# Performance work log

Measured on AMD Instinct MI355X. Metric: run time of the kernel, lower is better.

## Reference

```python
import jax, jax.numpy as jnp
import numpy as np

TOKEN_NUM = 8
GCN = 16          # group_channel_num = d_model
D_INNER = 32      # expand * d_model
D_STATE = 16
D_CONV = 4
DT_RANK = 1       # ceil(d_model / 16)
GROUPS = 4        # GroupNorm groups
EPS = 1e-5


def setup_inputs() -> dict:
    key = jax.random.key(0)
    ks = jax.random.split(key, 8)
    g = lambda k, shape, scale: jax.random.normal(k, shape, jnp.float32) * scale
    d = {}
    d["x"] = jax.random.normal(ks[0], (2, 128, 128, 128), jnp.float32)
    d["conv_w"] = g(ks[1], (128, 128, 3, 3), 0.03)
    d["conv_b"] = jnp.zeros((128,), jnp.float32)
    d["gn_w"] = jnp.ones((128,), jnp.float32)
    d["gn_b"] = jnp.zeros((128,), jnp.float32)
    d["in_proj_w"] = g(ks[2], (2 * D_INNER, GCN), 0.25)
    d["conv1d_w"] = g(ks[3], (D_INNER, 1, D_CONV), 0.3)
    d["conv1d_b"] = jnp.zeros((D_INNER,), jnp.float32)
    d["x_proj_w"] = g(ks[4], (DT_RANK + 2 * D_STATE, D_INNER), 0.18)
    d["dt_proj_w"] = g(ks[5], (D_INNER, DT_RANK), 1.0)
    d["dt_proj_b"] = jnp.full((D_INNER,), -2.0, jnp.float32)  # softplus -> small positive dt
    d["A_log"] = jnp.tile(jnp.log(jnp.arange(1, D_STATE + 1, dtype=jnp.float32)), (D_INNER, 1))
    d["D"] = jnp.ones((D_INNER,), jnp.float32)
    d["out_proj_w"] = g(ks[6], (GCN, D_INNER), 0.18)
    return d


def _mamba(seq, in_proj_w, conv1d_w, conv1d_b, x_proj_w, dt_proj_w, dt_proj_b, A_log, D, out_proj_w):
    # seq: (N, L, d_model)
    xz = jnp.einsum('nld,ed->nle', seq, in_proj_w)          # (N, L, 2*d_inner)
    xi, z = jnp.split(xz, 2, axis=-1)
    # causal depthwise conv1d over L, kernel D_CONV, then SiLU
    xc = jax.lax.conv_general_dilated(
        xi.transpose(0, 2, 1), conv1d_w, (1,), ((D_CONV - 1, 0),),
        dimension_numbers=('NCH', 'OIH', 'NCH'), feature_group_count=D_INNER)
    xc = jax.nn.silu((xc + conv1d_b[None, :, None]).transpose(0, 2, 1))  # (N, L, d_inner)
    xdbl = jnp.einsum('nld,ed->nle', xc, x_proj_w)          # (N, L, dt_rank+2*d_state)
    dt, Bm, Cm = jnp.split(xdbl, [DT_RANK, DT_RANK + D_STATE], axis=-1)
    dt = jax.nn.softplus(jnp.einsum('nlr,dr->nld', dt, dt_proj_w) + dt_proj_b)  # (N, L, d_inner)
    A = -jnp.exp(A_log)                                     # (d_inner, d_state)
    dA = jnp.exp(dt[..., None] * A)                         # (N, L, d_inner, d_state)
    dBx = dt[..., None] * Bm[:, :, None, :] * xc[..., None] # (N, L, d_inner, d_state)

    def step(h, inp):
        a, b, c = inp                                       # (N,d,s),(N,d,s),(N,s)
        h = a * h + b
        return h, jnp.sum(h * c[:, None, :], axis=-1)       # y_t: (N, d_inner)

    h0 = jnp.zeros((seq.shape[0], D_INNER, D_STATE), dA.dtype)
    _, ys = jax.lax.scan(step, h0, (dA.transpose(1, 0, 2, 3),
                                    dBx.transpose(1, 0, 2, 3),
                                    Cm.transpose(1, 0, 2)))
    ym = ys.transpose(1, 0, 2) + D * xc                     # skip connection D*x
    ym = ym * jax.nn.silu(z)                                # gate
    return jnp.einsum('nld,ed->nle', ym, out_proj_w)        # (N, L, d_model)


def reference(x, conv_w, conv_b, gn_w, gn_b, in_proj_w, conv1d_w, conv1d_b,
              x_proj_w, dt_proj_w, dt_proj_b, A_log, D, out_proj_w):
    B, C, H, W = x.shape
    # channels == channel_num so padding_feature is identity; 3x3 conv, pad 1
    y = jax.lax.conv_general_dilated(x, conv_w, (1, 1), ((1, 1), (1, 1)),
                                     dimension_numbers=('NCHW', 'OIHW', 'NCHW'))
    y = y + conv_b[None, :, None, None]
    seq = y.reshape(B * H * W, TOKEN_NUM, GCN)              # row-major view, matches torch .view
    out = _mamba(seq, in_proj_w, conv1d_w, conv1d_b, x_proj_w,
                 dt_proj_w, dt_proj_b, A_log, D, out_proj_w)
    xr = out.reshape(B, C, H, W)
    # GroupNorm(GROUPS, C) + SiLU
    g = xr.reshape(B, GROUPS, C // GROUPS, H, W)
    mu = g.mean((2, 3, 4), keepdims=True)
    var = g.var((2, 3, 4), keepdims=True)
    g = (g - mu) / jnp.sqrt(var + EPS)
    xp = g.reshape(B, C, H, W) * gn_w[None, :, None, None] + gn_b[None, :, None, None]
    xp = jax.nn.silu(xp)
    return x + xp
```

## Files before the change

kernel.cpp:

```cpp
#include <hip/hip_runtime.h>

typedef unsigned short USHORT;
typedef short short8 __attribute__((ext_vector_type(8)));
typedef float f32x4 __attribute__((ext_vector_type(4)));

__device__ __forceinline__ float fast_sig(float x) {
  return __builtin_amdgcn_rcpf(1.f + __builtin_amdgcn_exp2f(x * -1.442695041f));
}
__device__ __forceinline__ USHORT f2b(float f) {
  unsigned int u = __float_as_uint(f);
  unsigned int r = (u + 0x7fffu + ((u >> 16) & 1u)) >> 16;
  return (USHORT)r;
}
__device__ __forceinline__ void wave_lds_fence() {
  asm volatile("s_waitcnt lgkmcnt(0)" ::: "memory");
  __builtin_amdgcn_sched_barrier(0);
}

__global__ __launch_bounds__(256) void prep_k(
    const float* __restrict__ x, const float* __restrict__ cw,
    const float* __restrict__ w_in, const float* __restrict__ xpw,
    const float* __restrict__ wout,
    USHORT* __restrict__ xt_g, USHORT* __restrict__ wrep,
    USHORT* __restrict__ wbf) {
  const int tid = threadIdx.x;
  const int bid = blockIdx.x;
  if (bid < 2048) {
    __shared__ USHORT lt[128 * 18];
    const int cqi = bid & 7;
    const int h   = (bid >> 3) & 127;
    const int b   = bid >> 10;
    const int ci0 = cqi * 16;
#pragma unroll
    for (int it = 0; it < 2; ++it) {
      int task = it * 256 + tid;
      int ci = task >> 5;
      int wq = task & 31;
      float4 v = ((const float4*)(x + ((size_t)((b * 128 + ci0 + ci) * 128 + h)) * 128))[wq];
      lt[(wq * 4 + 0) * 18 + ci] = f2b(v.x);
      lt[(wq * 4 + 1) * 18 + ci] = f2b(v.y);
      lt[(wq * 4 + 2) * 18 + ci] = f2b(v.z);
      lt[(wq * 4 + 3) * 18 + ci] = f2b(v.w);
    }
    __syncthreads();
    unsigned int* dst = (unsigned int*)xt_g + ((size_t)((b * 128 + h) * 128)) * 64 + cqi * 8;
#pragma unroll
    for (int it = 0; it < 4; ++it) {
      int task = it * 256 + tid;
      int w = task >> 3;
      int p = task & 7;
      dst[(size_t)w * 64 + p] = *(const unsigned int*)&lt[w * 18 + 2 * p];
    }
  } else if (bid < 2624) {
    const int idx = (bid - 2048) * 256 + tid;
    const int t9 = idx % 9;
    const int r  = idx / 9;
    const int ci = r & 127;
    const int co = r >> 7;
    const int c  = ci >> 5;
    const int kg = (ci >> 3) & 3;
    const int j  = ci & 7;
    const int st = co >> 4;
    const int mm = co & 15;
    wrep[((c * 9 + t9) * 8 + st) * 512 + (kg * 16 + mm) * 8 + j] = f2b(cw[idx]);
  } else {
#pragma unroll
    for (int it = 0; it < 11; ++it) {
      int idx = it * 256 + tid;
      if (idx < 1024)      wbf[idx] = f2b(w_in[idx]);
      else if (idx < 2080) wbf[idx] = f2b(xpw[idx - 1024]);
      else if (idx < 2592) wbf[idx] = f2b(wout[idx - 2080]);
    }
  }
}

__global__ __launch_bounds__(512) void conv_mfma_k(
    const USHORT* __restrict__ xt_g, const USHORT* __restrict__ wrep,
    const float* __restrict__ cb, float* __restrict__ y) {
  __shared__ USHORT xt[3 * 136 * 136];

  const int tid = threadIdx.x;
  const int bid = blockIdx.x;
  const int h   = bid & 127;
  const int b   = bid >> 7;

  const int wv   = tid >> 6;
  const int lane = tid & 63;
  const int m    = lane & 15;
  const int kg   = lane >> 4;
  const int ch2  = wv & 1;
  const int co0w = ch2 * 64;
  const int ws0  = (wv >> 1) * 32;

  for (int it = 0; it < 13; ++it) {
    int task = it * 512 + tid;
    if (task < 6528) {
      int dh  = task / 2176;
      int rem = task - dh * 2176;
      int wl  = rem >> 4;
      int cq  = task & 15;
      int wg  = wl - 4;
      int hh  = h + dh - 1;
      uint4 v = make_uint4(0u, 0u, 0u, 0u);
      if (((unsigned)wg < 128u) && ((unsigned)hh < 128u))
        v = *(const uint4*)(xt_g + ((size_t)((b * 128 + hh) * 128 + wg)) * 128 + cq * 8);
      *(uint4*)&xt[(dh * 136 + wl) * 136 + cq * 8] = v;
    }
  }
  __syncthreads();

  f32x4 acc[4][2];
#pragma unroll
  for (int s = 0; s < 4; ++s)
#pragma unroll
    for (int ws = 0; ws < 2; ++ws) acc[s][ws] = (f32x4){0.f, 0.f, 0.f, 0.f};

  for (int c = 0; c < 4; ++c) {
#pragma unroll
    for (int t9 = 0; t9 < 9; ++t9) {
      const int kh = t9 / 3, kw = t9 - kh * 3;
      const USHORT* wbase = wrep + (size_t)(((c * 9 + t9) * 8 + ch2 * 4) * 512) + lane * 8;
      short8 a[4];
#pragma unroll
      for (int s = 0; s < 4; ++s)
        a[s] = *(const short8*)(wbase + s * 512);
#pragma unroll
      for (int ws = 0; ws < 2; ++ws) {
        short8 bf = *(const short8*)&xt[(kh * 136 + ws0 + ws * 16 + m + kw + 3) * 136 + c * 32 + kg * 8];
#pragma unroll
        for (int s = 0; s < 4; ++s)
          acc[s][ws] = __builtin_amdgcn_mfma_f32_16x16x32_bf16(a[s], bf, acc[s][ws], 0, 0, 0);
      }
    }
  }

#pragma unroll
  for (int s = 0; s < 4; ++s) {
#pragma unroll
    for (int ws = 0; ws < 2; ++ws) {
      const int w = ws0 + ws * 16 + m;
#pragma unroll
      for (int r = 0; r < 4; ++r) {
        const int co = co0w + s * 16 + kg * 4 + r;
        y[((size_t)((b * 128 + co) * 128 + h)) * 128 + w] = acc[s][ws][r] + cb[co];
      }
    }
  }
}

__global__ __launch_bounds__(256) void mamba_k(
    const float* __restrict__ y,
    const float* __restrict__ c1w, const float* __restrict__ c1b,
    const float* __restrict__ dtw, const float* __restrict__ dtb,
    const float* __restrict__ alog, const float* __restrict__ dvec,
    const USHORT* __restrict__ wbf,
    float* __restrict__ m, float* __restrict__ stats_part) {
  __shared__ float axs[64 * 36];
  __shared__ float azs[64 * 36];
  __shared__ USHORT ab[64 * 40];
  __shared__ float dt0s[64];
  __shared__ float Bs[64 * 16];
  __shared__ float Cs[64 * 16];
  __shared__ float reds[8];

  const int tid  = threadIdx.x;
  const int s    = tid >> 5;
  const int ch   = tid & 31;
  const int lane = tid & 63;
  const int wv   = tid >> 6;
  const int m15  = lane & 15;
  const int kg   = lane >> 4;

  const USHORT* w_inb = wbf;
  const USHORT* xpwb  = wbf + 1024;
  const USHORT* woutb = wbf + 2080;

  {
    short8 zero8 = (short8){0, 0, 0, 0, 0, 0, 0, 0};
    short8 a = zero8, b0 = zero8, b1 = zero8, b2 = zero8, b3 = zero8;
    if (kg < 2) {
      const int tok = wv * 16 + m15;
      const float* ya = y + (size_t)blockIdx.x * 1024 + (tok >> 3) * 128 + (tok & 7) * 16 + kg * 8;
      float4 f0 = *(const float4*)(ya);
      float4 f1 = *(const float4*)(ya + 4);
      a[0] = (short)f2b(f0.x); a[1] = (short)f2b(f0.y); a[2] = (short)f2b(f0.z); a[3] = (short)f2b(f0.w);
      a[4] = (short)f2b(f1.x); a[5] = (short)f2b(f1.y); a[6] = (short)f2b(f1.z); a[7] = (short)f2b(f1.w);
      b0 = *(const short8*)&w_inb[(0 * 16 + m15) * 16 + kg * 8];
      b1 = *(const short8*)&w_inb[(1 * 16 + m15) * 16 + kg * 8];
      b2 = *(const short8*)&w_inb[(2 * 16 + m15) * 16 + kg * 8];
      b3 = *(const short8*)&w_inb[(3 * 16 + m15) * 16 + kg * 8];
    }
    f32x4 zero = (f32x4){0.f, 0.f, 0.f, 0.f};
    f32x4 d0 = __builtin_amdgcn_mfma_f32_16x16x32_bf16(a, b0, zero, 0, 0, 0);
    f32x4 d1 = __builtin_amdgcn_mfma_f32_16x16x32_bf16(a, b1, zero, 0, 0, 0);
    f32x4 d2 = __builtin_amdgcn_mfma_f32_16x16x32_bf16(a, b2, zero, 0, 0, 0);
    f32x4 d3 = __builtin_amdgcn_mfma_f32_16x16x32_bf16(a, b3, zero, 0, 0, 0);
#pragma unroll
    for (int r = 0; r < 4; ++r) {
      const int tok = wv * 16 + kg * 4 + r;
      axs[tok * 36 + m15]      = d0[r];
      axs[tok * 36 + 16 + m15] = d1[r];
      azs[tok * 36 + m15]      = d2[r];
      azs[tok * 36 + 16 + m15] = d3[r];
    }
  }
  wave_lds_fence();

  const float4 cwv = *(const float4*)(c1w + ch * 4);
  const float cbr = c1b[ch];
  const float dwv = dtw[ch], dbv = dtb[ch], Dv = dvec[ch];
  float xc[8], zs[8];
  {
    float ax[8];
#pragma unroll
    for (int l = 0; l < 8; ++l) ax[l] = axs[(s * 8 + l) * 36 + ch];
#pragma unroll
    for (int l = 0; l < 8; ++l) {
      float a = fmaf(cwv.w, ax[l], cbr);
      if (l >= 1) a = fmaf(cwv.z, ax[l - 1], a);
      if (l >= 2) a = fmaf(cwv.y, ax[l - 2], a);
      if (l >= 3) a = fmaf(cwv.x, ax[l - 3], a);
      float sc = a * fast_sig(a);
      xc[l] = sc;
      ab[(s * 8 + l) * 40 + ch] = f2b(sc);
      float az = azs[(s * 8 + l) * 36 + ch];
      zs[l] = az * fast_sig(az);
    }
  }
  wave_lds_fence();

  {
    short8 a = *(const short8*)&ab[(wv * 16 + m15) * 40 + kg * 8];
    short8 b0 = *(const short8*)&xpwb[(0 * 16 + m15) * 32 + kg * 8];
    short8 b1 = *(const short8*)&xpwb[(1 * 16 + m15) * 32 + kg * 8];
    short8 b2;
    if (m15 == 0) b2 = *(const short8*)&xpwb[32 * 32 + kg * 8];
    else          b2 = (short8){0, 0, 0, 0, 0, 0, 0, 0};
    f32x4 zero = (f32x4){0.f, 0.f, 0.f, 0.f};
    f32x4 c0 = __builtin_amdgcn_mfma_f32_16x16x32_bf16(a, b0, zero, 0, 0, 0);
    f32x4 c1 = __builtin_amdgcn_mfma_f32_16x16x32_bf16(a, b1, zero, 0, 0, 0);
    f32x4 c2 = __builtin_amdgcn_mfma_f32_16x16x32_bf16(a, b2, zero, 0, 0, 0);
#pragma unroll
    for (int r = 0; r < 4; ++r) {
      const int tok = wv * 16 + kg * 4 + r;
      if (m15 == 0) {
        dt0s[tok] = c0[r];
        Bs[tok * 16 + 15] = c1[r];
        Cs[tok * 16 + 15] = c2[r];
      } else {
        Bs[tok * 16 + (m15 - 1)] = c0[r];
        Cs[tok * 16 + (m15 - 1)] = c1[r];
      }
    }
  }
  wave_lds_fence();

  float A2r[16];
#pragma unroll
  for (int q = 0; q < 4; ++q) {
    float4 av = ((const float4*)(alog + ch * 16))[q];
    A2r[q * 4 + 0] = -__builtin_amdgcn_exp2f(av.x * 1.442695041f) * 1.442695041f;
    A2r[q * 4 + 1] = -__builtin_amdgcn_exp2f(av.y * 1.442695041f) * 1.442695041f;
    A2r[q * 4 + 2] = -__builtin_amdgcn_exp2f(av.z * 1.442695041f) * 1.442695041f;
    A2r[q * 4 + 3] = -__builtin_amdgcn_exp2f(av.w * 1.442695041f) * 1.442695041f;
  }
  float hreg[16];
#pragma unroll
  for (int st = 0; st < 16; ++st) hreg[st] = 0.f;
#pragma unroll
  for (int l = 0; l < 8; ++l) {
    const int tok = s * 8 + l;
    float pre = fmaf(dt0s[tok], dwv, dbv);
    float t = __builtin_amdgcn_exp2f(pre * 1.442695041f);
    float dtl = 0.6931471806f * __builtin_amdgcn_logf(1.f + t);
    dtl = (pre > 20.f) ? pre : dtl;
    float dtxc = dtl * xc[l];
    float yl = 0.f;
#pragma unroll
    for (int q = 0; q < 4; ++q) {
      float4 bv = *(const float4*)&Bs[tok * 16 + q * 4];
      float4 cv = *(const float4*)&Cs[tok * 16 + q * 4];
      float aa;
      aa = __builtin_amdgcn_exp2f(dtl * A2r[q * 4 + 0]);
      hreg[q * 4 + 0] = fmaf(aa, hreg[q * 4 + 0], dtxc * bv.x);
      yl = fmaf(hreg[q * 4 + 0], cv.x, yl);
      aa = __builtin_amdgcn_exp2f(dtl * A2r[q * 4 + 1]);
      hreg[q * 4 + 1] = fmaf(aa, hreg[q * 4 + 1], dtxc * bv.y);
      yl = fmaf(hreg[q * 4 + 1], cv.y, yl);
      aa = __builtin_amdgcn_exp2f(dtl * A2r[q * 4 + 2]);
      hreg[q * 4 + 2] = fmaf(aa, hreg[q * 4 + 2], dtxc * bv.z);
      yl = fmaf(hreg[q * 4 + 2], cv.z, yl);
      aa = __builtin_amdgcn_exp2f(dtl * A2r[q * 4 + 3]);
      hreg[q * 4 + 3] = fmaf(aa, hreg[q * 4 + 3], dtxc * bv.w);
      yl = fmaf(hreg[q * 4 + 3], cv.w, yl);
    }
    ab[tok * 40 + ch] = f2b(fmaf(Dv, xc[l], yl) * zs[l]);
  }
  wave_lds_fence();

  float ls = 0.f, lq = 0.f;
  {
    short8 a2 = *(const short8*)&ab[(wv * 16 + m15) * 40 + kg * 8];
    short8 bo = *(const short8*)&woutb[m15 * 32 + kg * 8];
    f32x4 zero = (f32x4){0.f, 0.f, 0.f, 0.f};
    f32x4 o = __builtin_amdgcn_mfma_f32_16x16x32_bf16(a2, bo, zero, 0, 0, 0);
#pragma unroll
    for (int r = 0; r < 4; ++r) {
      const int tok = wv * 16 + kg * 4 + r;
      const int n   = blockIdx.x * 8 + (tok >> 3);
      const int l   = tok & 7;
      float v = o[r];
      m[(size_t)n * 128 + l * 16 + m15] = v;
      ls += v;
      lq = fmaf(v, v, lq);
    }
  }
#pragma unroll
  for (int off = 32; off > 0; off >>= 1) {
    ls += __shfl_down(ls, off);
    lq += __shfl_down(lq, off);
  }
  if (lane == 0) { reds[wv * 2] = ls; reds[wv * 2 + 1] = lq; }
  __syncthreads();
  if (tid == 0) {
    float S = reds[0] + reds[2] + reds[4] + reds[6];
    float Q = reds[1] + reds[3] + reds[5] + reds[7];
    int n0 = blockIdx.x * 8;
    int bb = n0 >> 14;
    int cc = (n0 >> 7) & 127;
    int gg = cc >> 5;
    float* line = stats_part + (blockIdx.x & 63) * 16;
    atomicAdd(&line[(bb * 4 + gg) * 2 + 0], S);
    atomicAdd(&line[(bb * 4 + gg) * 2 + 1], Q);
  }
}

__global__ __launch_bounds__(256) void gn_silu_k(
    const float* __restrict__ x,
    const float* __restrict__ gnw, const float* __restrict__ gnb,
    const float* __restrict__ stats_part, float* __restrict__ out) {
  __shared__ float sSQ[2];
  const int tid  = threadIdx.x;
  const int idx0 = (blockIdx.x * 256 + tid) * 4;
  const int bb = idx0 >> 21;
  const int cc = (idx0 >> 14) & 127;
  const int gg = cc >> 5;
  const int j2 = (bb * 4 + gg) * 2;

  if (tid < 64) {
    float s = stats_part[tid * 16 + j2];
    float q = stats_part[tid * 16 + j2 + 1];
#pragma unroll
    for (int off = 32; off > 0; off >>= 1) {
      s += __shfl_down(s, off);
      q += __shfl_down(q, off);
    }
    if (tid == 0) { sSQ[0] = s; sSQ[1] = q; }
  }
  __syncthreads();
  const float S = sSQ[0];
  const float Q = sSQ[1];
  const float inv  = 1.0f / 524288.0f;
  const float mu   = S * inv;
  const float var  = fmaf(Q, inv, -mu * mu);
  const float rstd = rsqrtf(var + 1e-5f);
  const float gw  = gnw[cc] * rstd;
  const float gb2 = gnb[cc] - mu * gw;

  float4 mv = *(const float4*)(out + idx0);
  float4 xv = *(const float4*)(x + idx0);
  float mvv[4] = { mv.x, mv.y, mv.z, mv.w };
  float xf[4]  = { xv.x, xv.y, xv.z, xv.w };
  float res[4];
#pragma unroll
  for (int j = 0; j < 4; ++j) {
    float nv = fmaf(mvv[j], gw, gb2);
    float sv = nv * fast_sig(nv);
    res[j] = xf[j] + sv;
  }
  *(float4*)(out + idx0) = make_float4(res[0], res[1], res[2], res[3]);
}

extern "C" void kernel_launch(void* const* d_in, const int* in_sizes, int n_in,
                              void* d_out, int out_size, void* d_ws, size_t ws_size,
                              hipStream_t stream) {
  const float* x     = (const float*)d_in[0];
  const float* convw = (const float*)d_in[1];
  const float* convb = (const float*)d_in[2];
  const float* gnw   = (const float*)d_in[3];
  const float* gnb   = (const float*)d_in[4];
  const float* winp  = (const float*)d_in[5];
  const float* c1w   = (const float*)d_in[6];
  const float* c1b   = (const float*)d_in[7];
  const float* xpw   = (const float*)d_in[8];
  const float* dtw   = (const float*)d_in[9];
  const float* dtb   = (const float*)d_in[10];
  const float* alog  = (const float*)d_in[11];
  const float* dvec  = (const float*)d_in[12];
  const float* wout  = (const float*)d_in[13];

  float*  y     = (float*)d_ws;
  float*  stats_part  = y + 4194304;
  USHORT* wbf   = (USHORT*)(stats_part + 1024);
  USHORT* xt_g  = (USHORT*)d_out;
  USHORT* wrep  = (USHORT*)d_out + 4194304;
  float*  m     = (float*)d_out;

  hipMemsetAsync(stats_part, 0, 1024 * sizeof(float), stream);
  hipLaunchKernelGGL(prep_k, dim3(2625), dim3(256), 0, stream,
                     x, convw, winp, xpw, wout, xt_g, wrep, wbf);
  hipLaunchKernelGGL(conv_mfma_k, dim3(256), dim3(512), 0, stream, xt_g, wrep, convb, y);
  hipLaunchKernelGGL(mamba_k, dim3(4096), dim3(256), 0, stream,
                     y, c1w, c1b, dtw, dtb, alog, dvec, wbf, m, stats_part);
  hipLaunchKernelGGL(gn_silu_k, dim3(4096), dim3(256), 0, stream,
                     x, gnw, gnb, stats_part, (float*)d_out);
}
```

Measured before the change: 161.2 us.

## Use per-wave LDS buffers in mamba and per-block stat slots instead of atomics

The mamba kernel's shared memory is compacted into two per-wave regions that are reused across stages (x/z projections, B/C/dt, bf16 activations), which reduces the LDS footprint and may let more blocks fit per CU. The GroupNorm statistics are no longer accumulated with atomics into a memset buffer. Each block now writes its sum and sum of squares to its own slot, and gn_silu reduces the 512 slots of its group. This removes the memset launch and atomic contention, but every gn_silu block repeats the 512-slot reduction.

```diff
diff --git a/kernel.cpp b/kernel.cpp
--- a/kernel.cpp
+++ b/kernel.cpp
@@ -154,13 +154,9 @@
     const float* __restrict__ dtw, const float* __restrict__ dtb,
     const float* __restrict__ alog, const float* __restrict__ dvec,
     const USHORT* __restrict__ wbf,
-    float* __restrict__ m, float* __restrict__ stats_part) {
-  __shared__ float axs[64 * 36];
-  __shared__ float azs[64 * 36];
-  __shared__ USHORT ab[64 * 40];
-  __shared__ float dt0s[64];
-  __shared__ float Bs[64 * 16];
-  __shared__ float Cs[64 * 16];
+    float* __restrict__ m, float2* __restrict__ slots) {
+  __shared__ float smA[4 * 576];
+  __shared__ float smB[4 * 576];
   __shared__ float reds[8];
 
   const int tid  = threadIdx.x;
@@ -170,6 +166,10 @@
   const int wv   = tid >> 6;
   const int m15  = lane & 15;
   const int kg   = lane >> 4;
+
+  float* wA = &smA[wv * 576];
+  float* wB = &smB[wv * 576];
+  USHORT* abw = (USHORT*)wB;
 
   const USHORT* w_inb = wbf;
   const USHORT* xpwb  = wbf + 1024;
@@ -197,11 +197,11 @@
     f32x4 d3 = __builtin_amdgcn_mfma_f32_16x16x32_bf16(a, b3, zero, 0, 0, 0);
 #pragma unroll
     for (int r = 0; r < 4; ++r) {
-      const int tok = wv * 16 + kg * 4 + r;
-      axs[tok * 36 + m15]      = d0[r];
-      axs[tok * 36 + 16 + m15] = d1[r];
-      azs[tok * 36 + m15]      = d2[r];
-      azs[tok * 36 + 16 + m15] = d3[r];
+      const int t = kg * 4 + r;
+      wA[t * 36 + m15]      = d0[r];
+      wA[t * 36 + 16 + m15] = d1[r];
+      wB[t * 36 + m15]      = d2[r];
+      wB[t * 36 + 16 + m15] = d3[r];
     }
   }
   wave_lds_fence();
@@ -211,9 +211,14 @@
   const float dwv = dtw[ch], dbv = dtb[ch], Dv = dvec[ch];
   float xc[8], zs[8];
   {
-    float ax[8];
-#pragma unroll
-    for (int l = 0; l < 8; ++l) ax[l] = axs[(s * 8 + l) * 36 + ch];
+    float ax[8], az[8];
+    const int tb = (s & 1) * 8;
+#pragma unroll
+    for (int l = 0; l < 8; ++l) {
+      ax[l] = wA[(tb + l) * 36 + ch];
+      az[l] = wB[(tb + l) * 36 + ch];
+    }
+    wave_lds_fence();
 #pragma unroll
     for (int l = 0; l < 8; ++l) {
       float a = fmaf(cwv.w, ax[l], cbr);
@@ -222,15 +227,14 @@
       if (l >= 3) a = fmaf(cwv.x, ax[l - 3], a);
       float sc = a * fast_sig(a);
       xc[l] = sc;
-      ab[(s * 8 + l) * 40 + ch] = f2b(sc);
-      float az = azs[(s * 8 + l) * 36 + ch];
-      zs[l] = az * fast_sig(az);
+      abw[(tb + l) * 40 + ch] = f2b(sc);
+      zs[l] = az[l] * fast_sig(az[l]);
     }
   }
   wave_lds_fence();
 
   {
-    short8 a = *(const short8*)&ab[(wv * 16 + m15) * 40 + kg * 8];
+    short8 a = *(const short8*)&abw[m15 * 40 + kg * 8];
     short8 b0 = *(const short8*)&xpwb[(0 * 16 + m15) * 32 + kg * 8];
     short8 b1 = *(const short8*)&xpwb[(1 * 16 + m15) * 32 + kg * 8];
     short8 b2;
@@ -242,14 +246,14 @@
     f32x4 c2 = __builtin_amdgcn_mfma_f32_16x16x32_bf16(a, b2, zero, 0, 0, 0);
 #pragma unroll
     for (int r = 0; r < 4; ++r) {
-      const int tok = wv * 16 + kg * 4 + r;
+      const int t = kg * 4 + r;
       if (m15 == 0) {
-        dt0s[tok] = c0[r];
-        Bs[tok * 16 + 15] = c1[r];
-        Cs[tok * 16 + 15] = c2[r];
+        wA[t]                 = c0[r];
+        wA[16 + t * 16 + 15]  = c1[r];
+        wA[272 + t * 16 + 15] = c2[r];
       } else {
-        Bs[tok * 16 + (m15 - 1)] = c0[r];
-        Cs[tok * 16 + (m15 - 1)] = c1[r];
+        wA[16 + t * 16 + (m15 - 1)]  = c0[r];
+        wA[272 + t * 16 + (m15 - 1)] = c1[r];
       }
     }
   }
@@ -267,40 +271,43 @@
   float hreg[16];
 #pragma unroll
   for (int st = 0; st < 16; ++st) hreg[st] = 0.f;
-#pragma unroll
-  for (int l = 0; l < 8; ++l) {
-    const int tok = s * 8 + l;
-    float pre = fmaf(dt0s[tok], dwv, dbv);
-    float t = __builtin_amdgcn_exp2f(pre * 1.442695041f);
-    float dtl = 0.6931471806f * __builtin_amdgcn_logf(1.f + t);
-    dtl = (pre > 20.f) ? pre : dtl;
-    float dtxc = dtl * xc[l];
-    float yl = 0.f;
-#pragma unroll
-    for (int q = 0; q < 4; ++q) {
-      float4 bv = *(const float4*)&Bs[tok * 16 + q * 4];
-      float4 cv = *(const float4*)&Cs[tok * 16 + q * 4];
-      float aa;
-      aa = __builtin_amdgcn_exp2f(dtl * A2r[q * 4 + 0]);
-      hreg[q * 4 + 0] = fmaf(aa, hreg[q * 4 + 0], dtxc * bv.x);
-      yl = fmaf(hreg[q * 4 + 0], cv.x, yl);
-      aa = __builtin_amdgcn_exp2f(dtl * A2r[q * 4 + 1]);
-      hreg[q * 4 + 1] = fmaf(aa, hreg[q * 4 + 1], dtxc * bv.y);
-      yl = fmaf(hreg[q * 4 + 1], cv.y, yl);
-      aa = __builtin_amdgcn_exp2f(dtl * A2r[q * 4 + 2]);
-      hreg[q * 4 + 2] = fmaf(aa, hreg[q * 4 + 2], dtxc * bv.z);
-      yl = fmaf(hreg[q * 4 + 2], cv.z, yl);
-      aa = __builtin_amdgcn_exp2f(dtl * A2r[q * 4 + 3]);
-      hreg[q * 4 + 3] = fmaf(aa, hreg[q * 4 + 3], dtxc * bv.w);
-      yl = fmaf(hreg[q * 4 + 3], cv.w, yl);
-    }
-    ab[tok * 40 + ch] = f2b(fmaf(Dv, xc[l], yl) * zs[l]);
+  {
+    const int tb = (s & 1) * 8;
+#pragma unroll
+    for (int l = 0; l < 8; ++l) {
+      const int t = tb + l;
+      float pre = fmaf(wA[t], dwv, dbv);
+      float tt = __builtin_amdgcn_exp2f(pre * 1.442695041f);
+      float dtl = 0.6931471806f * __builtin_amdgcn_logf(1.f + tt);
+      dtl = (pre > 20.f) ? pre : dtl;
+      float dtxc = dtl * xc[l];
+      float yl = 0.f;
+#pragma unroll
+      for (int q = 0; q < 4; ++q) {
+        float4 bv = *(const float4*)&wA[16 + t * 16 + q * 4];
+        float4 cv = *(const float4*)&wA[272 + t * 16 + q * 4];
+        float aa;
+        aa = __builtin_amdgcn_exp2f(dtl * A2r[q * 4 + 0]);
+        hreg[q * 4 + 0] = fmaf(aa, hreg[q * 4 + 0], dtxc * bv.x);
+        yl = fmaf(hreg[q * 4 + 0], cv.x, yl);
+        aa = __builtin_amdgcn_exp2f(dtl * A2r[q * 4 + 1]);
+        hreg[q * 4 + 1] = fmaf(aa, hreg[q * 4 + 1], dtxc * bv.y);
+        yl = fmaf(hreg[q * 4 + 1], cv.y, yl);
+        aa = __builtin_amdgcn_exp2f(dtl * A2r[q * 4 + 2]);
+        hreg[q * 4 + 2] = fmaf(aa, hreg[q * 4 + 2], dtxc * bv.z);
+        yl = fmaf(hreg[q * 4 + 2], cv.z, yl);
+        aa = __builtin_amdgcn_exp2f(dtl * A2r[q * 4 + 3]);
+        hreg[q * 4 + 3] = fmaf(aa, hreg[q * 4 + 3], dtxc * bv.w);
+        yl = fmaf(hreg[q * 4 + 3], cv.w, yl);
+      }
+      abw[t * 40 + ch] = f2b(fmaf(Dv, xc[l], yl) * zs[l]);
+    }
   }
   wave_lds_fence();
 
   float ls = 0.f, lq = 0.f;
   {
-    short8 a2 = *(const short8*)&ab[(wv * 16 + m15) * 40 + kg * 8];
+    short8 a2 = *(const short8*)&abw[m15 * 40 + kg * 8];
     short8 bo = *(const short8*)&woutb[m15 * 32 + kg * 8];
     f32x4 zero = (f32x4){0.f, 0.f, 0.f, 0.f};
     f32x4 o = __builtin_amdgcn_mfma_f32_16x16x32_bf16(a2, bo, zero, 0, 0, 0);
@@ -325,41 +332,35 @@
   if (tid == 0) {
     float S = reds[0] + reds[2] + reds[4] + reds[6];
     float Q = reds[1] + reds[3] + reds[5] + reds[7];
-    int n0 = blockIdx.x * 8;
-    int bb = n0 >> 14;
-    int cc = (n0 >> 7) & 127;
-    int gg = cc >> 5;
-    float* line = stats_part + (blockIdx.x & 63) * 16;
-    atomicAdd(&line[(bb * 4 + gg) * 2 + 0], S);
-    atomicAdd(&line[(bb * 4 + gg) * 2 + 1], Q);
+    slots[blockIdx.x] = make_float2(S, Q);
   }
 }
 
 __global__ __launch_bounds__(256) void gn_silu_k(
     const float* __restrict__ x,
     const float* __restrict__ gnw, const float* __restrict__ gnb,
-    const float* __restrict__ stats_part, float* __restrict__ out) {
-  __shared__ float sSQ[2];
+    const float2* __restrict__ slots, float* __restrict__ out) {
+  __shared__ float sred[8];
   const int tid  = threadIdx.x;
-  const int idx0 = (blockIdx.x * 256 + tid) * 4;
-  const int bb = idx0 >> 21;
+  const int bid  = blockIdx.x;
+  const int idx0 = (bid * 256 + tid) * 4;
   const int cc = (idx0 >> 14) & 127;
-  const int gg = cc >> 5;
-  const int j2 = (bb * 4 + gg) * 2;
-
-  if (tid < 64) {
-    float s = stats_part[tid * 16 + j2];
-    float q = stats_part[tid * 16 + j2 + 1];
+  const int g  = bid >> 9;
+
+  {
+    float2 p0 = slots[g * 512 + tid];
+    float2 p1 = slots[g * 512 + 256 + tid];
+    float s = p0.x + p1.x, q = p0.y + p1.y;
 #pragma unroll
     for (int off = 32; off > 0; off >>= 1) {
       s += __shfl_down(s, off);
       q += __shfl_down(q, off);
     }
-    if (tid == 0) { sSQ[0] = s; sSQ[1] = q; }
+    if ((tid & 63) == 0) { sred[(tid >> 6) * 2] = s; sred[(tid >> 6) * 2 + 1] = q; }
   }
   __syncthreads();
-  const float S = sSQ[0];
-  const float Q = sSQ[1];
+  const float S = sred[0] + sred[2] + sred[4] + sred[6];
+  const float Q = sred[1] + sred[3] + sred[5] + sred[7];
   const float inv  = 1.0f / 524288.0f;
   const float mu   = S * inv;
   const float var  = fmaf(Q, inv, -mu * mu);
@@ -400,18 +401,17 @@
   const float* wout  = (const float*)d_in[13];
 
   float*  y     = (float*)d_ws;
-  float*  stats_part  = y + 4194304;
-  USHORT* wbf   = (USHORT*)(stats_part + 1024);
+  float2* slots = (float2*)(y + 4194304);
+  USHORT* wbf   = (USHORT*)(slots + 4096);
   USHORT* xt_g  = (USHORT*)d_out;
   USHORT* wrep  = (USHORT*)d_out + 4194304;
   float*  m     = (float*)d_out;
 
-  hipMemsetAsync(stats_part, 0, 1024 * sizeof(float), stream);
   hipLaunchKernelGGL(prep_k, dim3(2625), dim3(256), 0, stream,
                      x, convw, winp, xpw, wout, xt_g, wrep, wbf);
   hipLaunchKernelGGL(conv_mfma_k, dim3(256), dim3(512), 0, stream, xt_g, wrep, convb, y);
   hipLaunchKernelGGL(mamba_k, dim3(4096), dim3(256), 0, stream,
-                     y, c1w, c1b, dtw, dtb, alog, dvec, wbf, m, stats_part);
+                     y, c1w, c1b, dtw, dtb, alog, dvec, wbf, m, slots);
   hipLaunchKernelGGL(gn_silu_k, dim3(4096), dim3(256), 0, stream,
-                     x, gnw, gnb, stats_part, (float*)d_out);
-}
+                     x, gnw, gnb, slots, (float*)d_out);
+}
```

Result: no change. 158.5 us (-1.7%).
